# Performance work log

Hardware: AMD Instinct MI355X
Metric: run time of the kernel (lower is better)

The kernel has to match this reference:

```python
import jax, jax.numpy as jnp
import numpy as np

# H36M-style 17-joint skeleton: bones[b] = (parent_joint, child_joint)
BONES = [(0,1),(1,2),(2,3),(0,4),(4,5),(5,6),(0,7),(7,8),(8,9),(9,10),
         (8,11),(11,12),(12,13),(8,14),(14,15),(15,16)]
N_JOINTS = 17
ROOT = 0


def _euler_xyz_to_matrix(e):
    # pytorch3d euler_angles_to_matrix(e, 'XYZ'): R = Rx(a) @ Ry(b) @ Rz(c)
    cx, cy, cz = jnp.cos(e[..., 0]), jnp.cos(e[..., 1]), jnp.cos(e[..., 2])
    sx, sy, sz = jnp.sin(e[..., 0]), jnp.sin(e[..., 1]), jnp.sin(e[..., 2])
    one, zero = jnp.ones_like(cx), jnp.zeros_like(cx)
    shp = e.shape[:-1] + (3, 3)
    Rx = jnp.stack([one, zero, zero, zero, cx, -sx, zero, sx, cx], -1).reshape(shp)
    Ry = jnp.stack([cy, zero, sy, zero, one, zero, -sy, zero, cy], -1).reshape(shp)
    Rz = jnp.stack([cz, -sz, zero, sz, cz, zero, zero, zero, one], -1).reshape(shp)
    return Rx @ Ry @ Rz


def setup_inputs() -> dict:
    key = jax.random.key(0)
    k1, k2 = jax.random.split(key)
    N = 500000
    euler_angle = jax.random.normal(k1, (N, 16, 3), dtype=jnp.float32)
    bone_length = jax.random.uniform(k2, (N, 16, 1), dtype=jnp.float32)
    return {"euler_angle": euler_angle, "bone_length": bone_length}


def reference(euler_angle, bone_length):
    # euler_angle: (N, 16, 3), bone_length: (N, 16, 1)
    N = euler_angle.shape[0]
    R = _euler_xyz_to_matrix(euler_angle)  # (N, 16, 3, 3)
    # Accumulated rotations in pytorch3d row-vector convention: p' = p @ M,
    # compose(M_parent, R_i) -> M_parent @ R_i.
    M = [None] * N_JOINTS
    pos = [None] * N_JOINTS
    M[ROOT] = jnp.broadcast_to(jnp.eye(3, dtype=euler_angle.dtype), (N, 3, 3))
    pos[ROOT] = jnp.zeros((N, 3), dtype=euler_angle.dtype)
    for i, (j0, j1) in enumerate(BONES):
        M[j1] = jnp.einsum('nij,njk->nik', M[j0], R[:, i])
        # local offset is (0, 0, L) so p @ M == L * M[:, 2, :] (third row)
        pos[j1] = bone_length[:, i, 0, None] * M[j1][:, 2, :] + pos[j0]
    return jnp.stack(pos, axis=1)  # (N, 17, 3)
```

## Files before the change

### kernel.cpp

```cpp
#include <hip/hip_runtime.h>


#define NB 64

#define GLB_PTR(x) ((const __attribute__((address_space(1))) void*)(x))
#define LDS_PTR(x) ((__attribute__((address_space(3))) void*)(x))

__device__ __forceinline__ void mm3(const float A[9], const float B[9], float C[9]) {
#pragma unroll
    for (int r = 0; r < 3; ++r) {
        C[3*r+0] = A[3*r+0]*B[0] + A[3*r+1]*B[3] + A[3*r+2]*B[6];
        C[3*r+1] = A[3*r+0]*B[1] + A[3*r+1]*B[4] + A[3*r+2]*B[7];
        C[3*r+2] = A[3*r+0]*B[2] + A[3*r+1]*B[5] + A[3*r+2]*B[8];
    }
}

__device__ __forceinline__ void erot(float a, float b, float c, float R[9]) {
    float sx, cx, sy, cy, sz, cz;
    __sincosf(a, &sx, &cx);
    __sincosf(b, &sy, &cy);
    __sincosf(c, &sz, &cz);
    R[0] = cy*cz;             R[1] = -cy*sz;            R[2] = sy;
    R[3] = sx*sy*cz + cx*sz;  R[4] = -sx*sy*sz + cx*cz; R[5] = -sx*cy;
    R[6] = -cx*sy*cz + sx*sz; R[7] = cx*sy*sz + sx*cz;  R[8] = cx*cy;
}

__global__ void __launch_bounds__(NB, 3)
fk17_kernel(const float* __restrict__ euler, const float* __restrict__ blen,
            float* __restrict__ out, int n)
{
    __shared__ float s_b[NB * 52];

    const int tid    = threadIdx.x;
    const int block0 = blockIdx.x * NB;
    const int nvalid = min(NB, n - block0);
    const int t      = block0 + tid;
    const int tc     = min(t, n - 1);

#pragma unroll
    for (int j = 0; j < 13; ++j) {
        int m = j * 64 + tid;
        int s = m / 13;
        int c = m - s * 13;
        if (c == 12) c = 0;
        int gs = min(block0 + s, n - 1);
        __builtin_amdgcn_global_load_lds(
            GLB_PTR(euler + (size_t)gs * 48 + c * 4),
            LDS_PTR(s_b + j * 256), 16, 0, 0);
    }

    float L[16];
    {
        const float4* gb4 = (const float4*)(blen + (size_t)tc * 16);
#pragma unroll
        for (int q = 0; q < 4; ++q) {
            float4 v = gb4[q];
            L[4*q+0] = v.x; L[4*q+1] = v.y; L[4*q+2] = v.z; L[4*q+3] = v.w;
        }
    }

    asm volatile("s_waitcnt vmcnt(0)" ::: "memory");
    __syncthreads();

    if (tid < nvalid) {
        float* o = s_b + tid * 52;
        float ex, ey, ez, fx, fy, fz;
        float Ma[9], Mb[9], M8[9], R[9];
        float px, py, pz, p8x, p8y, p8z;

        ex = o[0];  ey = o[1];  ez = o[2];
        fx = o[3];  fy = o[4];  fz = o[5];
        o[0] = 0.f; o[1] = 0.f; o[2] = 0.f;

        erot(ex, ey, ez, Ma);
        px = L[0]*Ma[6]; py = L[0]*Ma[7]; pz = L[0]*Ma[8];
        ex = o[6];  ey = o[7];  ez = o[8];
        o[3] = px; o[4] = py; o[5] = pz;
        erot(fx, fy, fz, R); mm3(Ma, R, Mb);
        px += L[1]*Mb[6]; py += L[1]*Mb[7]; pz += L[1]*Mb[8];
        fx = o[9];  fy = o[10]; fz = o[11];
        o[6] = px; o[7] = py; o[8] = pz;
        erot(ex, ey, ez, R); mm3(Mb, R, Ma);
        px += L[2]*Ma[6]; py += L[2]*Ma[7]; pz += L[2]*Ma[8];
        ex = o[12]; ey = o[13]; ez = o[14];
        o[9] = px; o[10] = py; o[11] = pz;

        erot(fx, fy, fz, Ma);
        px = L[3]*Ma[6]; py = L[3]*Ma[7]; pz = L[3]*Ma[8];
        fx = o[15]; fy = o[16]; fz = o[17];
        o[12] = px; o[13] = py; o[14] = pz;
        erot(ex, ey, ez, R); mm3(Ma, R, Mb);
        px += L[4]*Mb[6]; py += L[4]*Mb[7]; pz += L[4]*Mb[8];
        ex = o[18]; ey = o[19]; ez = o[20];
        o[15] = px; o[16] = py; o[17] = pz;
        erot(fx, fy, fz, R); mm3(Mb, R, Ma);
        px += L[5]*Ma[6]; py += L[5]*Ma[7]; pz += L[5]*Ma[8];
        fx = o[21]; fy = o[22]; fz = o[23];
        o[18] = px; o[19] = py; o[20] = pz;

        erot(ex, ey, ez, Ma);
        px = L[6]*Ma[6]; py = L[6]*Ma[7]; pz = L[6]*Ma[8];
        ex = o[24]; ey = o[25]; ez = o[26];
        o[21] = px; o[22] = py; o[23] = pz;
        erot(fx, fy, fz, R); mm3(Ma, R, M8);
        px += L[7]*M8[6]; py += L[7]*M8[7]; pz += L[7]*M8[8];
        fx = o[27]; fy = o[28]; fz = o[29];
        o[24] = px; o[25] = py; o[26] = pz;
        p8x = px; p8y = py; p8z = pz;

        erot(ex, ey, ez, R); mm3(M8, R, Ma);
        px = p8x + L[8]*Ma[6]; py = p8y + L[8]*Ma[7]; pz = p8z + L[8]*Ma[8];
        ex = o[30]; ey = o[31]; ez = o[32];
        o[27] = px; o[28] = py; o[29] = pz;
        erot(fx, fy, fz, R); mm3(Ma, R, Mb);
        px += L[9]*Mb[6]; py += L[9]*Mb[7]; pz += L[9]*Mb[8];
        fx = o[33]; fy = o[34]; fz = o[35];
        o[30] = px; o[31] = py; o[32] = pz;

        erot(ex, ey, ez, R); mm3(M8, R, Ma);
        px = p8x + L[10]*Ma[6]; py = p8y + L[10]*Ma[7]; pz = p8z + L[10]*Ma[8];
        ex = o[36]; ey = o[37]; ez = o[38];
        o[33] = px; o[34] = py; o[35] = pz;
        erot(fx, fy, fz, R); mm3(Ma, R, Mb);
        px += L[11]*Mb[6]; py += L[11]*Mb[7]; pz += L[11]*Mb[8];
        fx = o[39]; fy = o[40]; fz = o[41];
        o[36] = px; o[37] = py; o[38] = pz;
        erot(ex, ey, ez, R); mm3(Mb, R, Ma);
        px += L[12]*Ma[6]; py += L[12]*Ma[7]; pz += L[12]*Ma[8];
        ex = o[42]; ey = o[43]; ez = o[44];
        o[39] = px; o[40] = py; o[41] = pz;

        erot(fx, fy, fz, R); mm3(M8, R, Ma);
        px = p8x + L[13]*Ma[6]; py = p8y + L[13]*Ma[7]; pz = p8z + L[13]*Ma[8];
        fx = o[45]; fy = o[46]; fz = o[47];
        o[42] = px; o[43] = py; o[44] = pz;
        erot(ex, ey, ez, R); mm3(Ma, R, Mb);
        px += L[14]*Mb[6]; py += L[14]*Mb[7]; pz += L[14]*Mb[8];
        o[45] = px; o[46] = py; o[47] = pz;
        erot(fx, fy, fz, R); mm3(Mb, R, Ma);
        px += L[15]*Ma[6]; py += L[15]*Ma[7]; pz += L[15]*Ma[8];
        o[48] = px; o[49] = py; o[50] = pz;
    }
    __syncthreads();

    {
        float* og = out + (size_t)block0 * 51;
        if (nvalid == NB) {
#pragma unroll
            for (int k = 0; k < 51; ++k) {
                int m = tid + 64 * k;
                int s = m / 51;
                og[m] = s_b[m + s];
            }
        } else {
            const int tot = nvalid * 51;
            for (int m = tid; m < tot; m += NB) {
                int s = m / 51;
                og[m] = s_b[m + s];
            }
        }
    }
}

extern "C" void kernel_launch(void* const* d_in, const int* in_sizes, int n_in,
                              void* d_out, int out_size, void* d_ws, size_t ws_size,
                              hipStream_t stream) {
    const float* euler = (const float*)d_in[0];
    const float* blen  = (const float*)d_in[1];
    float* out = (float*)d_out;

    const int n    = in_sizes[0] / 48;
    const int grid = (n + NB - 1) / NB;
    fk17_kernel<<<grid, NB, 0, stream>>>(euler, blen, out, n);
}
```

Baseline: 200.3 us.

## Process multiple tiles per block with double-buffered LDS prefetch

Each block now loops over several 64-sample tiles. While the current tile is computed and written out, the next tile's euler angles are loaded asynchronously into a second LDS buffer and its bone lengths into registers, with partial vmcnt waits. The goal is to hide global load latency behind compute and to amortise per-block setup. The cost is a grid about five times smaller, leaving only a few waves per CU for latency hiding. The min-blocks hint in the launch bounds is also dropped, and correctness across tiles relies on single-wavefront ordering, since there is no barrier between iterations.

```diff
diff --git a/kernel.cpp b/kernel.cpp
--- a/kernel.cpp
+++ b/kernel.cpp
@@ -2,6 +2,7 @@
 
 
 #define NB 64
+#define KTILES 5
 
 #define GLB_PTR(x) ((const __attribute__((address_space(1))) void*)(x))
 #define LDS_PTR(x) ((__attribute__((address_space(3))) void*)(x))
@@ -25,140 +26,179 @@
     R[6] = -cx*sy*cz + sx*sz; R[7] = cx*sy*sz + sx*cz;  R[8] = cx*cy;
 }
 
-__global__ void __launch_bounds__(NB, 3)
+__device__ __forceinline__ void compute_tile(float* o, const float* L) {
+    float ex, ey, ez, fx, fy, fz;
+    float Ma[9], Mb[9], M8[9], R[9];
+    float px, py, pz, p8x, p8y, p8z;
+
+    ex = o[0];  ey = o[1];  ez = o[2];
+    fx = o[3];  fy = o[4];  fz = o[5];
+    o[0] = 0.f; o[1] = 0.f; o[2] = 0.f;
+
+    erot(ex, ey, ez, Ma);
+    px = L[0]*Ma[6]; py = L[0]*Ma[7]; pz = L[0]*Ma[8];
+    ex = o[6];  ey = o[7];  ez = o[8];
+    o[3] = px; o[4] = py; o[5] = pz;
+    erot(fx, fy, fz, R); mm3(Ma, R, Mb);
+    px += L[1]*Mb[6]; py += L[1]*Mb[7]; pz += L[1]*Mb[8];
+    fx = o[9];  fy = o[10]; fz = o[11];
+    o[6] = px; o[7] = py; o[8] = pz;
+    erot(ex, ey, ez, R); mm3(Mb, R, Ma);
+    px += L[2]*Ma[6]; py += L[2]*Ma[7]; pz += L[2]*Ma[8];
+    ex = o[12]; ey = o[13]; ez = o[14];
+    o[9] = px; o[10] = py; o[11] = pz;
+
+    erot(fx, fy, fz, Ma);
+    px = L[3]*Ma[6]; py = L[3]*Ma[7]; pz = L[3]*Ma[8];
+    fx = o[15]; fy = o[16]; fz = o[17];
+    o[12] = px; o[13] = py; o[14] = pz;
+    erot(ex, ey, ez, R); mm3(Ma, R, Mb);
+    px += L[4]*Mb[6]; py += L[4]*Mb[7]; pz += L[4]*Mb[8];
+    ex = o[18]; ey = o[19]; ez = o[20];
+    o[15] = px; o[16] = py; o[17] = pz;
+    erot(fx, fy, fz, R); mm3(Mb, R, Ma);
+    px += L[5]*Ma[6]; py += L[5]*Ma[7]; pz += L[5]*Ma[8];
+    fx = o[21]; fy = o[22]; fz = o[23];
+    o[18] = px; o[19] = py; o[20] = pz;
+
+    erot(ex, ey, ez, Ma);
+    px = L[6]*Ma[6]; py = L[6]*Ma[7]; pz = L[6]*Ma[8];
+    ex = o[24]; ey = o[25]; ez = o[26];
+    o[21] = px; o[22] = py; o[23] = pz;
+    erot(fx, fy, fz, R); mm3(Ma, R, M8);
+    px += L[7]*M8[6]; py += L[7]*M8[7]; pz += L[7]*M8[8];
+    fx = o[27]; fy = o[28]; fz = o[29];
+    o[24] = px; o[25] = py; o[26] = pz;
+    p8x = px; p8y = py; p8z = pz;
+
+    erot(ex, ey, ez, R); mm3(M8, R, Ma);
+    px = p8x + L[8]*Ma[6]; py = p8y + L[8]*Ma[7]; pz = p8z + L[8]*Ma[8];
+    ex = o[30]; ey = o[31]; ez = o[32];
+    o[27] = px; o[28] = py; o[29] = pz;
+    erot(fx, fy, fz, R); mm3(Ma, R, Mb);
+    px += L[9]*Mb[6]; py += L[9]*Mb[7]; pz += L[9]*Mb[8];
+    fx = o[33]; fy = o[34]; fz = o[35];
+    o[30] = px; o[31] = py; o[32] = pz;
+
+    erot(ex, ey, ez, R); mm3(M8, R, Ma);
+    px = p8x + L[10]*Ma[6]; py = p8y + L[10]*Ma[7]; pz = p8z + L[10]*Ma[8];
+    ex = o[36]; ey = o[37]; ez = o[38];
+    o[33] = px; o[34] = py; o[35] = pz;
+    erot(fx, fy, fz, R); mm3(Ma, R, Mb);
+    px += L[11]*Mb[6]; py += L[11]*Mb[7]; pz += L[11]*Mb[8];
+    fx = o[39]; fy = o[40]; fz = o[41];
+    o[36] = px; o[37] = py; o[38] = pz;
+    erot(ex, ey, ez, R); mm3(Mb, R, Ma);
+    px += L[12]*Ma[6]; py += L[12]*Ma[7]; pz += L[12]*Ma[8];
+    ex = o[42]; ey = o[43]; ez = o[44];
+    o[39] = px; o[40] = py; o[41] = pz;
+
+    erot(fx, fy, fz, R); mm3(M8, R, Ma);
+    px = p8x + L[13]*Ma[6]; py = p8y + L[13]*Ma[7]; pz = p8z + L[13]*Ma[8];
+    fx = o[45]; fy = o[46]; fz = o[47];
+    o[42] = px; o[43] = py; o[44] = pz;
+    erot(ex, ey, ez, R); mm3(Ma, R, Mb);
+    px += L[14]*Mb[6]; py += L[14]*Mb[7]; pz += L[14]*Mb[8];
+    o[45] = px; o[46] = py; o[47] = pz;
+    erot(fx, fy, fz, R); mm3(Mb, R, Ma);
+    px += L[15]*Ma[6]; py += L[15]*Ma[7]; pz += L[15]*Ma[8];
+    o[48] = px; o[49] = py; o[50] = pz;
+}
+
+__global__ void __launch_bounds__(NB)
 fk17_kernel(const float* __restrict__ euler, const float* __restrict__ blen,
-            float* __restrict__ out, int n)
+            float* __restrict__ out, int n, int ntiles, int ktiles)
 {
-    __shared__ float s_b[NB * 52];
-
-    const int tid    = threadIdx.x;
-    const int block0 = blockIdx.x * NB;
-    const int nvalid = min(NB, n - block0);
-    const int t      = block0 + tid;
-    const int tc     = min(t, n - 1);
-
-#pragma unroll
-    for (int j = 0; j < 13; ++j) {
-        int m = j * 64 + tid;
-        int s = m / 13;
-        int c = m - s * 13;
-        if (c == 12) c = 0;
-        int gs = min(block0 + s, n - 1);
-        __builtin_amdgcn_global_load_lds(
-            GLB_PTR(euler + (size_t)gs * 48 + c * 4),
-            LDS_PTR(s_b + j * 256), 16, 0, 0);
-    }
-
-    float L[16];
+    __shared__ float s_b[2][NB * 52];
+
+    const int tid   = threadIdx.x;
+    const int tile0 = blockIdx.x * ktiles;
+    if (tile0 >= ntiles) return;
+    const int kc = min(ktiles, ntiles - tile0);
+
+    float Lc[16], Ln[16];
+
     {
+        const int t  = tile0 * NB + tid;
+        const int tc = min(t, n - 1);
         const float4* gb4 = (const float4*)(blen + (size_t)tc * 16);
 #pragma unroll
         for (int q = 0; q < 4; ++q) {
             float4 v = gb4[q];
-            L[4*q+0] = v.x; L[4*q+1] = v.y; L[4*q+2] = v.z; L[4*q+3] = v.w;
+            Lc[4*q+0] = v.x; Lc[4*q+1] = v.y; Lc[4*q+2] = v.z; Lc[4*q+3] = v.w;
+        }
+        const int base = tile0 * NB;
+#pragma unroll
+        for (int j = 0; j < 13; ++j) {
+            int m = j * 64 + tid;
+            int s = m / 13;
+            int c = m - s * 13;
+            if (c == 12) c = 0;
+            int gs = min(base + s, n - 1);
+            __builtin_amdgcn_global_load_lds(
+                GLB_PTR(euler + (size_t)gs * 48 + c * 4),
+                LDS_PTR(&s_b[0][0] + j * 256), 16, 0, 0);
         }
     }
 
-    asm volatile("s_waitcnt vmcnt(0)" ::: "memory");
-    __syncthreads();
-
-    if (tid < nvalid) {
-        float* o = s_b + tid * 52;
-        float ex, ey, ez, fx, fy, fz;
-        float Ma[9], Mb[9], M8[9], R[9];
-        float px, py, pz, p8x, p8y, p8z;
-
-        ex = o[0];  ey = o[1];  ez = o[2];
-        fx = o[3];  fy = o[4];  fz = o[5];
-        o[0] = 0.f; o[1] = 0.f; o[2] = 0.f;
-
-        erot(ex, ey, ez, Ma);
-        px = L[0]*Ma[6]; py = L[0]*Ma[7]; pz = L[0]*Ma[8];
-        ex = o[6];  ey = o[7];  ez = o[8];
-        o[3] = px; o[4] = py; o[5] = pz;
-        erot(fx, fy, fz, R); mm3(Ma, R, Mb);
-        px += L[1]*Mb[6]; py += L[1]*Mb[7]; pz += L[1]*Mb[8];
-        fx = o[9];  fy = o[10]; fz = o[11];
-        o[6] = px; o[7] = py; o[8] = pz;
-        erot(ex, ey, ez, R); mm3(Mb, R, Ma);
-        px += L[2]*Ma[6]; py += L[2]*Ma[7]; pz += L[2]*Ma[8];
-        ex = o[12]; ey = o[13]; ez = o[14];
-        o[9] = px; o[10] = py; o[11] = pz;
-
-        erot(fx, fy, fz, Ma);
-        px = L[3]*Ma[6]; py = L[3]*Ma[7]; pz = L[3]*Ma[8];
-        fx = o[15]; fy = o[16]; fz = o[17];
-        o[12] = px; o[13] = py; o[14] = pz;
-        erot(ex, ey, ez, R); mm3(Ma, R, Mb);
-        px += L[4]*Mb[6]; py += L[4]*Mb[7]; pz += L[4]*Mb[8];
-        ex = o[18]; ey = o[19]; ez = o[20];
-        o[15] = px; o[16] = py; o[17] = pz;
-        erot(fx, fy, fz, R); mm3(Mb, R, Ma);
-        px += L[5]*Ma[6]; py += L[5]*Ma[7]; pz += L[5]*Ma[8];
-        fx = o[21]; fy = o[22]; fz = o[23];
-        o[18] = px; o[19] = py; o[20] = pz;
-
-        erot(ex, ey, ez, Ma);
-        px = L[6]*Ma[6]; py = L[6]*Ma[7]; pz = L[6]*Ma[8];
-        ex = o[24]; ey = o[25]; ez = o[26];
-        o[21] = px; o[22] = py; o[23] = pz;
-        erot(fx, fy, fz, R); mm3(Ma, R, M8);
-        px += L[7]*M8[6]; py += L[7]*M8[7]; pz += L[7]*M8[8];
-        fx = o[27]; fy = o[28]; fz = o[29];
-        o[24] = px; o[25] = py; o[26] = pz;
-        p8x = px; p8y = py; p8z = pz;
-
-        erot(ex, ey, ez, R); mm3(M8, R, Ma);
-        px = p8x + L[8]*Ma[6]; py = p8y + L[8]*Ma[7]; pz = p8z + L[8]*Ma[8];
-        ex = o[30]; ey = o[31]; ez = o[32];
-        o[27] = px; o[28] = py; o[29] = pz;
-        erot(fx, fy, fz, R); mm3(Ma, R, Mb);
-        px += L[9]*Mb[6]; py += L[9]*Mb[7]; pz += L[9]*Mb[8];
-        fx = o[33]; fy = o[34]; fz = o[35];
-        o[30] = px; o[31] = py; o[32] = pz;
-
-        erot(ex, ey, ez, R); mm3(M8, R, Ma);
-        px = p8x + L[10]*Ma[6]; py = p8y + L[10]*Ma[7]; pz = p8z + L[10]*Ma[8];
-        ex = o[36]; ey = o[37]; ez = o[38];
-        o[33] = px; o[34] = py; o[35] = pz;
-        erot(fx, fy, fz, R); mm3(Ma, R, Mb);
-        px += L[11]*Mb[6]; py += L[11]*Mb[7]; pz += L[11]*Mb[8];
-        fx = o[39]; fy = o[40]; fz = o[41];
-        o[36] = px; o[37] = py; o[38] = pz;
-        erot(ex, ey, ez, R); mm3(Mb, R, Ma);
-        px += L[12]*Ma[6]; py += L[12]*Ma[7]; pz += L[12]*Ma[8];
-        ex = o[42]; ey = o[43]; ez = o[44];
-        o[39] = px; o[40] = py; o[41] = pz;
-
-        erot(fx, fy, fz, R); mm3(M8, R, Ma);
-        px = p8x + L[13]*Ma[6]; py = p8y + L[13]*Ma[7]; pz = p8z + L[13]*Ma[8];
-        fx = o[45]; fy = o[46]; fz = o[47];
-        o[42] = px; o[43] = py; o[44] = pz;
-        erot(ex, ey, ez, R); mm3(Ma, R, Mb);
-        px += L[14]*Mb[6]; py += L[14]*Mb[7]; pz += L[14]*Mb[8];
-        o[45] = px; o[46] = py; o[47] = pz;
-        erot(fx, fy, fz, R); mm3(Mb, R, Ma);
-        px += L[15]*Ma[6]; py += L[15]*Ma[7]; pz += L[15]*Ma[8];
-        o[48] = px; o[49] = py; o[50] = pz;
-    }
-    __syncthreads();
-
-    {
-        float* og = out + (size_t)block0 * 51;
-        if (nvalid == NB) {
-#pragma unroll
-            for (int k = 0; k < 51; ++k) {
-                int m = tid + 64 * k;
-                int s = m / 51;
-                og[m] = s_b[m + s];
+    for (int i = 0; i < kc; ++i) {
+        const int  cur  = i & 1;
+        float*     bb   = &s_b[cur][0];
+        const int  tile = tile0 + i;
+        const bool pf   = (i + 1 < kc);
+
+        if (pf) {
+            const int t  = (tile + 1) * NB + tid;
+            const int tc = min(t, n - 1);
+            const float4* gb4 = (const float4*)(blen + (size_t)tc * 16);
+#pragma unroll
+            for (int q = 0; q < 4; ++q) {
+                float4 v = gb4[q];
+                Ln[4*q+0] = v.x; Ln[4*q+1] = v.y; Ln[4*q+2] = v.z; Ln[4*q+3] = v.w;
             }
-        } else {
-            const int tot = nvalid * 51;
-            for (int m = tid; m < tot; m += NB) {
-                int s = m / 51;
-                og[m] = s_b[m + s];
+            const int base = (tile + 1) * NB;
+            float* nb = &s_b[cur ^ 1][0];
+#pragma unroll
+            for (int j = 0; j < 13; ++j) {
+                int m = j * 64 + tid;
+                int s = m / 13;
+                int c = m - s * 13;
+                if (c == 12) c = 0;
+                int gs = min(base + s, n - 1);
+                __builtin_amdgcn_global_load_lds(
+                    GLB_PTR(euler + (size_t)gs * 48 + c * 4),
+                    LDS_PTR(nb + j * 256), 16, 0, 0);
             }
         }
+
+        if (pf) asm volatile("s_waitcnt vmcnt(17)" ::: "memory");
+        else    asm volatile("s_waitcnt vmcnt(0)"  ::: "memory");
+        __builtin_amdgcn_sched_barrier(0);
+
+        const int nv = min(NB, n - tile * NB);
+        if (tid < nv) compute_tile(bb + tid * 52, Lc);
+
+        {
+            float* og = out + (size_t)tile * NB * 51;
+            if (nv == NB) {
+#pragma unroll
+                for (int k = 0; k < 51; ++k) {
+                    int m = tid + 64 * k;
+                    int s = m / 51;
+                    og[m] = bb[m + s];
+                }
+            } else {
+                const int tot = nv * 51;
+                for (int m = tid; m < tot; m += NB) {
+                    int s = m / 51;
+                    og[m] = bb[m + s];
+                }
+            }
+        }
+        __builtin_amdgcn_sched_barrier(0);
+
+#pragma unroll
+        for (int q = 0; q < 16; ++q) Lc[q] = Ln[q];
     }
 }
 
@@ -169,7 +209,8 @@
     const float* blen  = (const float*)d_in[1];
     float* out = (float*)d_out;
 
-    const int n    = in_sizes[0] / 48;
-    const int grid = (n + NB - 1) / NB;
-    fk17_kernel<<<grid, NB, 0, stream>>>(euler, blen, out, n);
-}
+    const int n      = in_sizes[0] / 48;
+    const int ntiles = (n + NB - 1) / NB;
+    const int grid   = (ntiles + KTILES - 1) / KTILES;
+    fk17_kernel<<<grid, NB, 0, stream>>>(euler, blen, out, n, ntiles, KTILES);
+}
```

Result: slower. 218.4 us (+9.0%).
